# Kernel tuning notes

Hardware: AMD Instinct MI355X
Metric: run time of the kernel (lower is better)

## Reference

```python
import jax, jax.numpy as jnp
import numpy as np

N_HEAD = 16
MASK_PENALTY = 10000.0


def setup_inputs() -> dict:
    key = jax.random.key(0)
    k1, k2, k3 = jax.random.split(key, 3)
    B, S, D = 2, 2048, 1024
    x = jax.random.normal(k1, (B, S, D), dtype=jnp.float32)
    w_attn = jax.random.normal(k2, (D, 3 * D), dtype=jnp.float32) * 0.02
    b_attn = jnp.zeros((3 * D,), dtype=jnp.float32)
    w_proj = jax.random.normal(k3, (D, D), dtype=jnp.float32) * 0.02
    b_proj = jnp.zeros((D,), dtype=jnp.float32)
    return {"x": x, "w_attn": w_attn, "b_attn": b_attn, "w_proj": w_proj, "b_proj": b_proj}


def _split_heads(t, n_head):
    B, S, D = t.shape
    return t.reshape(B, S, n_head, D // n_head).transpose(0, 2, 1, 3)  # [B,H,S,dh]


def reference(x, w_attn, b_attn, w_proj, b_proj):
    B, S, D = x.shape
    qkv = x @ w_attn + b_attn  # fused QKV conv1d: [B,S,3D]
    q, k, v = jnp.split(qkv, 3, axis=2)
    q = _split_heads(q, N_HEAD)
    k = _split_heads(k, N_HEAD)
    v = _split_heads(v, N_HEAD)
    dh = D // N_HEAD
    w = jnp.einsum("bhqd,bhkd->bhqk", q, k) / jnp.sqrt(jnp.asarray(dh, dtype=q.dtype))
    # GPT-2 additive causal mask: w*b - 10000*(1-b)
    i = jnp.arange(S)[:, None]
    j = jnp.arange(S)[None, :]
    b = (i >= j).astype(w.dtype)  # nd == ns here
    w = w * b - MASK_PENALTY * (1.0 - b)
    w = jax.nn.softmax(w, axis=-1)
    a = jnp.einsum("bhqk,bhkd->bhqd", w, v)  # [B,H,S,dh]
    a = a.transpose(0, 2, 1, 3).reshape(B, S, D)  # merge heads
    return a @ w_proj + b_proj
```

## Files before the change

### kernel.cpp

```cpp
#include <hip/hip_runtime.h>


typedef short short8 __attribute__((ext_vector_type(8)));
typedef float f32x4 __attribute__((ext_vector_type(4)));

__device__ __forceinline__ unsigned short f2b(float f) {
    unsigned int x;
    __builtin_memcpy(&x, &f, 4);
    unsigned int r = x + 0x7FFF + ((x >> 16) & 1);
    return (unsigned short)(r >> 16);
}

__device__ __forceinline__ void load_lds16(const unsigned short* g, unsigned short* l) {
    __builtin_amdgcn_global_load_lds(
        (const __attribute__((address_space(1))) unsigned int*)g,
        (__attribute__((address_space(3))) unsigned int*)l, 16, 0, 0);
}

__global__ __launch_bounds__(256) void xcast(const float* __restrict__ in,
                                             unsigned int* __restrict__ out) {
    int i = (blockIdx.x * 256 + threadIdx.x) * 4;
    float4 f = *(const float4*)(in + i);
    uint2 p;
    p.x = (unsigned int)f2b(f.x) | ((unsigned int)f2b(f.y) << 16);
    p.y = (unsigned int)f2b(f.z) | ((unsigned int)f2b(f.w) << 16);
    *(uint2*)(out + i / 2) = p;
}

__global__ __launch_bounds__(256) void transpose_k(const float* __restrict__ in,
                                                   unsigned short* __restrict__ out,
                                                   int R, int C) {
    __shared__ unsigned short t[32][33];
    int c0 = blockIdx.x * 32, r0 = blockIdx.y * 32;
    int tx = threadIdx.x, ty = threadIdx.y;
#pragma unroll
    for (int i = 0; i < 4; i++)
        t[ty + i * 8][tx] = f2b(in[(r0 + ty + i * 8) * C + c0 + tx]);
    __syncthreads();
#pragma unroll
    for (int i = 0; i < 4; i++)
        out[(c0 + ty + i * 8) * R + r0 + tx] = t[tx][ty + i * 8];
}

__global__ __launch_bounds__(256) void qkv_gemm(const unsigned short* __restrict__ X,
                                                const unsigned short* __restrict__ WT,
                                                const float* __restrict__ bias,
                                                unsigned short* __restrict__ Qo,
                                                unsigned short* __restrict__ Ko,
                                                unsigned short* __restrict__ Vt) {
    __shared__ __align__(16) unsigned short As[128 * 32];
    __shared__ __align__(16) unsigned short Bs[128 * 32];
    const int tid = threadIdx.x;
    const int w = tid >> 6, l = tid & 63, l15 = l & 15, quad = l >> 4;
    const int wr = w >> 1, wc = w & 1;
    const int m0 = blockIdx.y * 128, n0 = blockIdx.x * 128;

    const int sr = w * 16 + (l >> 2);
    const int gch = (l & 3) ^ ((l >> 3) & 3);
    const unsigned short* Asrc = X + (size_t)(m0 + sr) * 1024 + gch * 8;
    const unsigned short* Bsrc = WT + (size_t)(n0 + sr) * 1024 + gch * 8;
    const int rswz = (l15 >> 1) & 3;

    f32x4 acc[4][4];
#pragma unroll
    for (int mt = 0; mt < 4; mt++)
#pragma unroll
        for (int nt = 0; nt < 4; nt++) acc[mt][nt] = (f32x4){0.f, 0.f, 0.f, 0.f};

    for (int k0 = 0; k0 < 1024; k0 += 32) {
        __syncthreads();
        load_lds16(Asrc + k0, &As[tid * 8]);
        load_lds16(Asrc + 65536 + k0, &As[2048 + tid * 8]);
        load_lds16(Bsrc + k0, &Bs[tid * 8]);
        load_lds16(Bsrc + 65536 + k0, &Bs[2048 + tid * 8]);
        __syncthreads();

        short8 af[4], bfr[4];
#pragma unroll
        for (int mt = 0; mt < 4; mt++)
            af[mt] = *(const short8*)&As[(wr * 64 + mt * 16 + l15) * 32 + ((quad ^ rswz) * 8)];
#pragma unroll
        for (int nt = 0; nt < 4; nt++)
            bfr[nt] = *(const short8*)&Bs[(wc * 64 + nt * 16 + l15) * 32 + ((quad ^ rswz) * 8)];
#pragma unroll
        for (int mt = 0; mt < 4; mt++)
#pragma unroll
            for (int nt = 0; nt < 4; nt++)
                acc[mt][nt] = __builtin_amdgcn_mfma_f32_16x16x32_bf16(af[mt], bfr[nt], acc[mt][nt], 0, 0, 0);
    }

    const int which = n0 >> 10;
    float bv[4];
#pragma unroll
    for (int nt = 0; nt < 4; nt++) bv[nt] = bias[n0 + wc * 64 + nt * 16 + l15];

#pragma unroll
    for (int mt = 0; mt < 4; mt++)
#pragma unroll
        for (int nt = 0; nt < 4; nt++)
#pragma unroll
            for (int r = 0; r < 4; r++) {
                int mg = m0 + wr * 64 + mt * 16 + quad * 4 + r;
                int ng = n0 + wc * 64 + nt * 16 + l15;
                float v = acc[mt][nt][r] + bv[nt];
                int bb = mg >> 11, s = mg & 2047;
                int c = ng & 1023, h = c >> 6, d = c & 63;
                size_t slab = (size_t)(bb * 16 + h);
                if (which == 0)      Qo[(slab * 2048 + s) * 64 + d] = f2b(v);
                else if (which == 1) Ko[(slab * 2048 + s) * 64 + d] = f2b(v);
                else                 Vt[(slab * 64 + d) * 2048 + s] = f2b(v);
            }
}

__global__ __launch_bounds__(256) void attn_k(const unsigned short* __restrict__ Q,
                                              const unsigned short* __restrict__ K,
                                              const unsigned short* __restrict__ Vt,
                                              unsigned short* __restrict__ Om) {
    __shared__ __align__(16) unsigned short Qs[64 * 64];
    __shared__ __align__(16) unsigned short Ks[64 * 64];
    __shared__ __align__(16) unsigned short Vts[64 * 64];
    __shared__ __align__(16) unsigned short Ps[64][72];

    const int tid = threadIdx.x;
    const int w = tid >> 6, l = tid & 63, l15 = l & 15, quad = l >> 4;
    const int bid = blockIdx.x;
    const int qt = 31 - (bid >> 5);
    const int hb = bid & 31;
    const int q0 = qt * 64;
    const unsigned short* Qb = Q + (size_t)hb * 131072;
    const unsigned short* Kb = K + (size_t)hb * 131072;
    const unsigned short* Vb = Vt + (size_t)hb * 131072;

    const int sr = w * 8 + (l >> 3);
    const int gch = (l & 7) ^ (l >> 3);
    const int swz = l15 & 7;

    load_lds16(Qb + (q0 + sr) * 64 + gch * 8, &Qs[tid * 8]);
    load_lds16(Qb + (q0 + 32 + sr) * 64 + gch * 8, &Qs[2048 + tid * 8]);
    __syncthreads();

    short8 qf[2];
#pragma unroll
    for (int ks = 0; ks < 2; ks++)
        qf[ks] = *(const short8*)&Qs[(w * 16 + l15) * 64 + (((ks * 4 + quad) ^ swz) * 8)];

    f32x4 o[4];
    float l_i[4];
#pragma unroll
    for (int nt = 0; nt < 4; nt++) o[nt] = (f32x4){0.f, 0.f, 0.f, 0.f};
#pragma unroll
    for (int r = 0; r < 4; r++) l_i[r] = 0.f;

    for (int kt = 0; kt <= qt; kt++) {
        const int k0 = kt * 64;
        __syncthreads();
        load_lds16(Kb + (k0 + sr) * 64 + gch * 8, &Ks[tid * 8]);
        load_lds16(Kb + (k0 + 32 + sr) * 64 + gch * 8, &Ks[2048 + tid * 8]);
        load_lds16(Vb + sr * 2048 + k0 + gch * 8, &Vts[tid * 8]);
        load_lds16(Vb + (32 + sr) * 2048 + k0 + gch * 8, &Vts[2048 + tid * 8]);
        __syncthreads();

        f32x4 sa[4];
#pragma unroll
        for (int nt = 0; nt < 4; nt++) sa[nt] = (f32x4){0.f, 0.f, 0.f, 0.f};
#pragma unroll
        for (int ks = 0; ks < 2; ks++)
#pragma unroll
            for (int nt = 0; nt < 4; nt++) {
                short8 kf = *(const short8*)&Ks[(nt * 16 + l15) * 64 + (((ks * 4 + quad) ^ swz) * 8)];
                sa[nt] = __builtin_amdgcn_mfma_f32_16x16x32_bf16(qf[ks], kf, sa[nt], 0, 0, 0);
            }

        float pv[4][4];
        if (kt == qt) {
#pragma unroll
            for (int nt = 0; nt < 4; nt++)
#pragma unroll
                for (int r = 0; r < 4; r++) {
                    bool ok = (nt * 16 + l15) <= (w * 16 + quad * 4 + r);
                    pv[nt][r] = ok ? __expf(sa[nt][r] * 0.125f) : 0.f;
                }
        } else {
#pragma unroll
            for (int nt = 0; nt < 4; nt++)
#pragma unroll
                for (int r = 0; r < 4; r++)
                    pv[nt][r] = __expf(sa[nt][r] * 0.125f);
        }
#pragma unroll
        for (int r = 0; r < 4; r++)
            l_i[r] += (pv[0][r] + pv[1][r]) + (pv[2][r] + pv[3][r]);

#pragma unroll
        for (int nt = 0; nt < 4; nt++)
#pragma unroll
            for (int r = 0; r < 4; r++)
                Ps[w * 16 + quad * 4 + r][nt * 16 + l15] = f2b(pv[nt][r]);

        asm volatile("s_waitcnt lgkmcnt(0)" ::: "memory");

#pragma unroll
        for (int ks = 0; ks < 2; ks++) {
            short8 pf = *(const short8*)&Ps[w * 16 + l15][ks * 32 + quad * 8];
#pragma unroll
            for (int nt = 0; nt < 4; nt++) {
                short8 vf = *(const short8*)&Vts[(nt * 16 + l15) * 64 + (((ks * 4 + quad) ^ swz) * 8)];
                o[nt] = __builtin_amdgcn_mfma_f32_16x16x32_bf16(pf, vf, o[nt], 0, 0, 0);
            }
        }
    }

#pragma unroll
    for (int r = 0; r < 4; r++) {
        float s = l_i[r];
        s += __shfl_xor(s, 1, 64);
        s += __shfl_xor(s, 2, 64);
        s += __shfl_xor(s, 4, 64);
        s += __shfl_xor(s, 8, 64);
        l_i[r] = 1.0f / s;
    }
    const int b = hb >> 4, h = hb & 15;
#pragma unroll
    for (int nt = 0; nt < 4; nt++)
#pragma unroll
        for (int r = 0; r < 4; r++) {
            int sg = q0 + w * 16 + quad * 4 + r;
            int col = h * 64 + nt * 16 + l15;
            Om[((size_t)(b * 2048 + sg)) * 1024 + col] = f2b(o[nt][r] * l_i[r]);
        }
}

__global__ __launch_bounds__(256) void proj_gemm(const unsigned short* __restrict__ A,
                                                 const unsigned short* __restrict__ WT,
                                                 const float* __restrict__ bias,
                                                 float* __restrict__ out) {
    __shared__ __align__(16) unsigned short As[128 * 32];
    __shared__ __align__(16) unsigned short Bs[64 * 32];
    const int tid = threadIdx.x;
    const int w = tid >> 6, l = tid & 63, l15 = l & 15, quad = l >> 4;
    const int wr = w >> 1, wc = w & 1;
    const int m0 = blockIdx.y * 128, n0 = blockIdx.x * 64;

    const int sr = w * 16 + (l >> 2);
    const int gch = (l & 3) ^ ((l >> 3) & 3);
    const unsigned short* Asrc = A + (size_t)(m0 + sr) * 1024 + gch * 8;
    const unsigned short* Bsrc = WT + (size_t)(n0 + sr) * 1024 + gch * 8;
    const int rswz = (l15 >> 1) & 3;

    f32x4 acc[4][2];
#pragma unroll
    for (int mt = 0; mt < 4; mt++)
#pragma unroll
        for (int nt = 0; nt < 2; nt++) acc[mt][nt] = (f32x4){0.f, 0.f, 0.f, 0.f};

    for (int k0 = 0; k0 < 1024; k0 += 32) {
        __syncthreads();
        load_lds16(Asrc + k0, &As[tid * 8]);
        load_lds16(Asrc + 65536 + k0, &As[2048 + tid * 8]);
        load_lds16(Bsrc + k0, &Bs[tid * 8]);
        __syncthreads();

        short8 af[4], bfr[2];
#pragma unroll
        for (int mt = 0; mt < 4; mt++)
            af[mt] = *(const short8*)&As[(wr * 64 + mt * 16 + l15) * 32 + ((quad ^ rswz) * 8)];
#pragma unroll
        for (int nt = 0; nt < 2; nt++)
            bfr[nt] = *(const short8*)&Bs[(wc * 32 + nt * 16 + l15) * 32 + ((quad ^ rswz) * 8)];
#pragma unroll
        for (int mt = 0; mt < 4; mt++)
#pragma unroll
            for (int nt = 0; nt < 2; nt++)
                acc[mt][nt] = __builtin_amdgcn_mfma_f32_16x16x32_bf16(af[mt], bfr[nt], acc[mt][nt], 0, 0, 0);
    }

#pragma unroll
    for (int mt = 0; mt < 4; mt++)
#pragma unroll
        for (int nt = 0; nt < 2; nt++)
#pragma unroll
            for (int r = 0; r < 4; r++) {
                int mg = m0 + wr * 64 + mt * 16 + quad * 4 + r;
                int ng = n0 + wc * 32 + nt * 16 + l15;
                out[(size_t)mg * 1024 + ng] = acc[mt][nt][r] + bias[ng];
            }
}

extern "C" void kernel_launch(void* const* d_in, const int* in_sizes, int n_in,
                              void* d_out, int out_size, void* d_ws, size_t ws_size,
                              hipStream_t stream) {
    (void)in_sizes; (void)n_in; (void)out_size; (void)ws_size;
    const float* x      = (const float*)d_in[0];
    const float* w_attn = (const float*)d_in[1];
    const float* b_attn = (const float*)d_in[2];
    const float* w_proj = (const float*)d_in[3];
    const float* b_proj = (const float*)d_in[4];
    float* out = (float*)d_out;
    unsigned short* ws = (unsigned short*)d_ws;

    unsigned short* wtA  = ws;
    unsigned short* wtP  = wtA + 3145728;
    unsigned short* Qw   = wtP + 1048576;
    unsigned short* Kw   = Qw + 4194304;
    unsigned short* Vtw  = Kw + 4194304;
    unsigned short* XbOm = Vtw + 4194304;

    xcast<<<4096, 256, 0, stream>>>(x, (unsigned int*)XbOm);
    transpose_k<<<dim3(96, 32), dim3(32, 8), 0, stream>>>(w_attn, wtA, 1024, 3072);
    transpose_k<<<dim3(32, 32), dim3(32, 8), 0, stream>>>(w_proj, wtP, 1024, 1024);
    qkv_gemm<<<dim3(24, 32), 256, 0, stream>>>(XbOm, wtA, b_attn, Qw, Kw, Vtw);
    attn_k<<<1024, 256, 0, stream>>>(Qw, Kw, Vtw, XbOm);
    proj_gemm<<<dim3(16, 32), 256, 0, stream>>>(XbOm, wtP, b_proj, out);
}
```

Baseline: 190.0 us.

## Double-buffer attention K/V, fuse prep kernels, stage V-transpose stores through LDS

Merges the x cast and two weight transposes into one launch. The QKV GEMM epilogue folds the 1/sqrt(dh) scale into K and writes the transposed V through swizzled LDS so global stores become coalesced 16-byte writes. The attention kernel double-buffers K/V tiles so the next tile's loads overlap the current tile's compute, and reuses the Q buffer for P. The row sum is computed with an MFMA against a ones vector instead of shuffle reductions. These add LDS use and reduce row-sum precision because P is summed after rounding to bf16.

```diff
diff --git a/kernel.cpp b/kernel.cpp
--- a/kernel.cpp
+++ b/kernel.cpp
@@ -1,4 +1,5 @@
 #include <hip/hip_runtime.h>
+#include <hip/hip_bf16.h>
 
 
 typedef short short8 __attribute__((ext_vector_type(8)));
@@ -11,28 +12,40 @@
     return (unsigned short)(r >> 16);
 }
 
+__device__ __forceinline__ unsigned int pk2(float a, float b) {
+    __hip_bfloat162 h = __float22bfloat162_rn(make_float2(a, b));
+    unsigned int u;
+    __builtin_memcpy(&u, &h, 4);
+    return u;
+}
+
 __device__ __forceinline__ void load_lds16(const unsigned short* g, unsigned short* l) {
     __builtin_amdgcn_global_load_lds(
         (const __attribute__((address_space(1))) unsigned int*)g,
         (__attribute__((address_space(3))) unsigned int*)l, 16, 0, 0);
 }
 
-__global__ __launch_bounds__(256) void xcast(const float* __restrict__ in,
-                                             unsigned int* __restrict__ out) {
-    int i = (blockIdx.x * 256 + threadIdx.x) * 4;
-    float4 f = *(const float4*)(in + i);
-    uint2 p;
-    p.x = (unsigned int)f2b(f.x) | ((unsigned int)f2b(f.y) << 16);
-    p.y = (unsigned int)f2b(f.z) | ((unsigned int)f2b(f.w) << 16);
-    *(uint2*)(out + i / 2) = p;
-}
-
-__global__ __launch_bounds__(256) void transpose_k(const float* __restrict__ in,
-                                                   unsigned short* __restrict__ out,
-                                                   int R, int C) {
+__global__ __launch_bounds__(256) void prep(const float* __restrict__ x, unsigned int* __restrict__ xb,
+                                            const float* __restrict__ wA, unsigned short* __restrict__ wtA,
+                                            const float* __restrict__ wP, unsigned short* __restrict__ wtP) {
+    const int bx = blockIdx.x, tid = threadIdx.x;
+    if (bx < 4096) {
+        int i = (bx * 256 + tid) * 4;
+        float4 f = *(const float4*)(x + i);
+        uint2 p;
+        p.x = (unsigned int)f2b(f.x) | ((unsigned int)f2b(f.y) << 16);
+        p.y = (unsigned int)f2b(f.z) | ((unsigned int)f2b(f.w) << 16);
+        *(uint2*)(xb + i / 2) = p;
+        return;
+    }
     __shared__ unsigned short t[32][33];
-    int c0 = blockIdx.x * 32, r0 = blockIdx.y * 32;
-    int tx = threadIdx.x, ty = threadIdx.y;
+    const float* in;
+    unsigned short* out;
+    int R, C, gx, gy;
+    if (bx < 7168) { int i = bx - 4096; gx = i % 96; gy = i / 96; in = wA; out = wtA; R = 1024; C = 3072; }
+    else           { int i = bx - 7168; gx = i % 32; gy = i / 32; in = wP; out = wtP; R = 1024; C = 1024; }
+    const int tx = tid & 31, ty = tid >> 5;
+    const int c0 = gx * 32, r0 = gy * 32;
 #pragma unroll
     for (int i = 0; i < 4; i++)
         t[ty + i * 8][tx] = f2b(in[(r0 + ty + i * 8) * C + c0 + tx]);
@@ -48,8 +61,9 @@
                                                 unsigned short* __restrict__ Qo,
                                                 unsigned short* __restrict__ Ko,
                                                 unsigned short* __restrict__ Vt) {
-    __shared__ __align__(16) unsigned short As[128 * 32];
-    __shared__ __align__(16) unsigned short Bs[128 * 32];
+    __shared__ __align__(16) unsigned short SMEM[8192];
+    unsigned short* As = SMEM;
+    unsigned short* Bs = SMEM + 4096;
     const int tid = threadIdx.x;
     const int w = tid >> 6, l = tid & 63, l15 = l & 15, quad = l >> 4;
     const int wr = w >> 1, wc = w & 1;
@@ -90,36 +104,65 @@
     }
 
     const int which = n0 >> 10;
+    const int c0 = n0 & 1023;
     float bv[4];
 #pragma unroll
     for (int nt = 0; nt < 4; nt++) bv[nt] = bias[n0 + wc * 64 + nt * 16 + l15];
 
-#pragma unroll
-    for (int mt = 0; mt < 4; mt++)
-#pragma unroll
-        for (int nt = 0; nt < 4; nt++)
-#pragma unroll
-            for (int r = 0; r < 4; r++) {
-                int mg = m0 + wr * 64 + mt * 16 + quad * 4 + r;
-                int ng = n0 + wc * 64 + nt * 16 + l15;
-                float v = acc[mt][nt][r] + bv[nt];
-                int bb = mg >> 11, s = mg & 2047;
-                int c = ng & 1023, h = c >> 6, d = c & 63;
-                size_t slab = (size_t)(bb * 16 + h);
-                if (which == 0)      Qo[(slab * 2048 + s) * 64 + d] = f2b(v);
-                else if (which == 1) Ko[(slab * 2048 + s) * 64 + d] = f2b(v);
-                else                 Vt[(slab * 64 + d) * 2048 + s] = f2b(v);
-            }
+    if (which < 2) {
+        const float scale = (which == 1) ? 0.125f : 1.0f;
+        unsigned short* dst = (which == 0) ? Qo : Ko;
+#pragma unroll
+        for (int mt = 0; mt < 4; mt++)
+#pragma unroll
+            for (int nt = 0; nt < 4; nt++)
+#pragma unroll
+                for (int r = 0; r < 4; r++) {
+                    int mg = m0 + wr * 64 + mt * 16 + quad * 4 + r;
+                    int cg = c0 + wc * 64 + nt * 16 + l15;
+                    float v = (acc[mt][nt][r] + bv[nt]) * scale;
+                    int h = cg >> 6, d = cg & 63;
+                    dst[(((size_t)(mg >> 11) * 16 + h) * 2048 + (mg & 2047)) * 64 + d] = f2b(v);
+                }
+    } else {
+        const int b = m0 >> 11, sbase = m0 & 2047, h0 = c0 >> 6;
+#pragma unroll
+        for (int p = 0; p < 2; p++) {
+            __syncthreads();
+            if (wc == p) {
+#pragma unroll
+                for (int mt = 0; mt < 4; mt++)
+#pragma unroll
+                    for (int nt = 0; nt < 4; nt++)
+#pragma unroll
+                        for (int r = 0; r < 4; r++) {
+                            float v = acc[mt][nt][r] + bv[nt];
+                            int d = nt * 16 + l15;
+                            int mloc = wr * 64 + mt * 16 + quad * 4 + r;
+                            SMEM[d * 128 + (((mloc >> 4) ^ (d & 7)) << 4) + (mloc & 15)] = f2b(v);
+                        }
+            }
+            __syncthreads();
+            const int d = tid >> 2, q4 = tid & 3;
+            size_t gb = ((size_t)((b * 16 + h0 + p) * 64 + d)) * 2048 + sbase + q4 * 32;
+#pragma unroll
+            for (int half = 0; half < 2; half++) {
+                int mc = q4 * 2 + half;
+                const uint4* s = (const uint4*)&SMEM[d * 128 + ((mc ^ (d & 7)) << 4)];
+                *(uint4*)(Vt + gb + half * 16) = s[0];
+                *(uint4*)(Vt + gb + half * 16 + 8) = s[1];
+            }
+        }
+    }
 }
 
 __global__ __launch_bounds__(256) void attn_k(const unsigned short* __restrict__ Q,
                                               const unsigned short* __restrict__ K,
                                               const unsigned short* __restrict__ Vt,
                                               unsigned short* __restrict__ Om) {
-    __shared__ __align__(16) unsigned short Qs[64 * 64];
-    __shared__ __align__(16) unsigned short Ks[64 * 64];
-    __shared__ __align__(16) unsigned short Vts[64 * 64];
-    __shared__ __align__(16) unsigned short Ps[64][72];
+    __shared__ __align__(16) unsigned short Ks[2][4096];
+    __shared__ __align__(16) unsigned short Vts[2][4096];
+    __shared__ __align__(16) unsigned short QP[4096];
 
     const int tid = threadIdx.x;
     const int w = tid >> 6, l = tid & 63, l15 = l & 15, quad = l >> 4;
@@ -135,30 +178,38 @@
     const int gch = (l & 7) ^ (l >> 3);
     const int swz = l15 & 7;
 
-    load_lds16(Qb + (q0 + sr) * 64 + gch * 8, &Qs[tid * 8]);
-    load_lds16(Qb + (q0 + 32 + sr) * 64 + gch * 8, &Qs[2048 + tid * 8]);
+    load_lds16(Qb + (q0 + sr) * 64 + gch * 8, &QP[tid * 8]);
+    load_lds16(Qb + (q0 + 32 + sr) * 64 + gch * 8, &QP[2048 + tid * 8]);
+    load_lds16(Kb + sr * 64 + gch * 8, &Ks[0][tid * 8]);
+    load_lds16(Kb + (32 + sr) * 64 + gch * 8, &Ks[0][2048 + tid * 8]);
+    load_lds16(Vb + sr * 2048 + gch * 8, &Vts[0][tid * 8]);
+    load_lds16(Vb + (32 + sr) * 2048 + gch * 8, &Vts[0][2048 + tid * 8]);
     __syncthreads();
 
     short8 qf[2];
 #pragma unroll
     for (int ks = 0; ks < 2; ks++)
-        qf[ks] = *(const short8*)&Qs[(w * 16 + l15) * 64 + (((ks * 4 + quad) ^ swz) * 8)];
-
-    f32x4 o[4];
-    float l_i[4];
+        qf[ks] = *(const short8*)&QP[(w * 16 + l15) * 64 + (((ks * 4 + quad) ^ swz) << 3)];
+
+    short8 ones;
+#pragma unroll
+    for (int j = 0; j < 8; j++) ones[j] = (short)0x3F80;
+
+    f32x4 o[4], lacc;
 #pragma unroll
     for (int nt = 0; nt < 4; nt++) o[nt] = (f32x4){0.f, 0.f, 0.f, 0.f};
-#pragma unroll
-    for (int r = 0; r < 4; r++) l_i[r] = 0.f;
+    lacc = (f32x4){0.f, 0.f, 0.f, 0.f};
 
     for (int kt = 0; kt <= qt; kt++) {
-        const int k0 = kt * 64;
-        __syncthreads();
-        load_lds16(Kb + (k0 + sr) * 64 + gch * 8, &Ks[tid * 8]);
-        load_lds16(Kb + (k0 + 32 + sr) * 64 + gch * 8, &Ks[2048 + tid * 8]);
-        load_lds16(Vb + sr * 2048 + k0 + gch * 8, &Vts[tid * 8]);
-        load_lds16(Vb + (32 + sr) * 2048 + k0 + gch * 8, &Vts[2048 + tid * 8]);
-        __syncthreads();
+        const int c = kt & 1;
+        __syncthreads();
+        if (kt < qt) {
+            const int kn = (kt + 1) * 64;
+            load_lds16(Kb + (kn + sr) * 64 + gch * 8, &Ks[1 - c][tid * 8]);
+            load_lds16(Kb + (kn + 32 + sr) * 64 + gch * 8, &Ks[1 - c][2048 + tid * 8]);
+            load_lds16(Vb + sr * 2048 + kn + gch * 8, &Vts[1 - c][tid * 8]);
+            load_lds16(Vb + (32 + sr) * 2048 + kn + gch * 8, &Vts[1 - c][2048 + tid * 8]);
+        }
 
         f32x4 sa[4];
 #pragma unroll
@@ -167,7 +218,7 @@
         for (int ks = 0; ks < 2; ks++)
 #pragma unroll
             for (int nt = 0; nt < 4; nt++) {
-                short8 kf = *(const short8*)&Ks[(nt * 16 + l15) * 64 + (((ks * 4 + quad) ^ swz) * 8)];
+                short8 kf = *(const short8*)&Ks[c][(nt * 16 + l15) * 64 + (((ks * 4 + quad) ^ swz) << 3)];
                 sa[nt] = __builtin_amdgcn_mfma_f32_16x16x32_bf16(qf[ks], kf, sa[nt], 0, 0, 0);
             }
 
@@ -178,47 +229,45 @@
 #pragma unroll
                 for (int r = 0; r < 4; r++) {
                     bool ok = (nt * 16 + l15) <= (w * 16 + quad * 4 + r);
-                    pv[nt][r] = ok ? __expf(sa[nt][r] * 0.125f) : 0.f;
+                    pv[nt][r] = ok ? __expf(sa[nt][r]) : 0.f;
                 }
         } else {
 #pragma unroll
             for (int nt = 0; nt < 4; nt++)
 #pragma unroll
                 for (int r = 0; r < 4; r++)
-                    pv[nt][r] = __expf(sa[nt][r] * 0.125f);
-        }
-#pragma unroll
-        for (int r = 0; r < 4; r++)
-            l_i[r] += (pv[0][r] + pv[1][r]) + (pv[2][r] + pv[3][r]);
-
-#pragma unroll
-        for (int nt = 0; nt < 4; nt++)
-#pragma unroll
-            for (int r = 0; r < 4; r++)
-                Ps[w * 16 + quad * 4 + r][nt * 16 + l15] = f2b(pv[nt][r]);
-
+                    pv[nt][r] = __expf(sa[nt][r]);
+        }
+
+        const int rb = w * 16 + quad * 4;
+#pragma unroll
+        for (int nt = 0; nt < 4; nt++) {
+            const int col = nt * 16 + l15, ch = col >> 3, wi = col & 7;
+#pragma unroll
+            for (int rp = 0; rp < 4; rp += 2) {
+                unsigned int u = pk2(pv[nt][rp], pv[nt][rp + 1]);
+                const int ra = rb + rp, rbn = ra + 1;
+                QP[ra * 64 + ((ch ^ (ra & 7)) << 3) + wi] = (unsigned short)(u & 0xffff);
+                QP[rbn * 64 + ((ch ^ (rbn & 7)) << 3) + wi] = (unsigned short)(u >> 16);
+            }
+        }
         asm volatile("s_waitcnt lgkmcnt(0)" ::: "memory");
 
 #pragma unroll
         for (int ks = 0; ks < 2; ks++) {
-            short8 pf = *(const short8*)&Ps[w * 16 + l15][ks * 32 + quad * 8];
+            short8 pf = *(const short8*)&QP[(w * 16 + l15) * 64 + (((ks * 4 + quad) ^ swz) << 3)];
+            lacc = __builtin_amdgcn_mfma_f32_16x16x32_bf16(pf, ones, lacc, 0, 0, 0);
 #pragma unroll
             for (int nt = 0; nt < 4; nt++) {
-                short8 vf = *(const short8*)&Vts[(nt * 16 + l15) * 64 + (((ks * 4 + quad) ^ swz) * 8)];
+                short8 vf = *(const short8*)&Vts[c][(nt * 16 + l15) * 64 + (((ks * 4 + quad) ^ swz) << 3)];
                 o[nt] = __builtin_amdgcn_mfma_f32_16x16x32_bf16(pf, vf, o[nt], 0, 0, 0);
             }
         }
     }
 
-#pragma unroll
-    for (int r = 0; r < 4; r++) {
-        float s = l_i[r];
-        s += __shfl_xor(s, 1, 64);
-        s += __shfl_xor(s, 2, 64);
-        s += __shfl_xor(s, 4, 64);
-        s += __shfl_xor(s, 8, 64);
-        l_i[r] = 1.0f / s;
-    }
+    float inv[4];
+#pragma unroll
+    for (int r = 0; r < 4; r++) inv[r] = 1.0f / lacc[r];
     const int b = hb >> 4, h = hb & 15;
 #pragma unroll
     for (int nt = 0; nt < 4; nt++)
@@ -226,7 +275,7 @@
         for (int r = 0; r < 4; r++) {
             int sg = q0 + w * 16 + quad * 4 + r;
             int col = h * 64 + nt * 16 + l15;
-            Om[((size_t)(b * 2048 + sg)) * 1024 + col] = f2b(o[nt][r] * l_i[r]);
+            Om[((size_t)(b * 2048 + sg)) * 1024 + col] = f2b(o[nt][r] * inv[r]);
         }
 }
 
@@ -305,9 +354,7 @@
     unsigned short* Vtw  = Kw + 4194304;
     unsigned short* XbOm = Vtw + 4194304;
 
-    xcast<<<4096, 256, 0, stream>>>(x, (unsigned int*)XbOm);
-    transpose_k<<<dim3(96, 32), dim3(32, 8), 0, stream>>>(w_attn, wtA, 1024, 3072);
-    transpose_k<<<dim3(32, 32), dim3(32, 8), 0, stream>>>(w_proj, wtP, 1024, 1024);
+    prep<<<8192, 256, 0, stream>>>(x, (unsigned int*)XbOm, w_attn, wtA, w_proj, wtP);
     qkv_gemm<<<dim3(24, 32), 256, 0, stream>>>(XbOm, wtA, b_attn, Qw, Kw, Vtw);
     attn_k<<<1024, 256, 0, stream>>>(Qw, Kw, Vtw, XbOm);
     proj_gemm<<<dim3(16, 32), 256, 0, stream>>>(XbOm, wtP, b_proj, out);
```

After: 189.8 us. Within noise of the previous version (-0.1%).
